# Kernel optimization log

Hardware: AMD Instinct MI355X
Metric: run time of the kernel (lower is better)

## Reference

```python
import jax, jax.numpy as jnp
import numpy as np

N = 50000       # num_node
E = 800000      # num edges (avg degree 32)
F_IN, F_HID, F_OUT = 128, 128, 64


def setup_inputs() -> dict:
    key = jax.random.key(0)
    ks = jax.random.split(key, 8)
    x = jax.random.normal(ks[0], (N, F_IN), dtype=jnp.float32)
    edge_index = jax.random.randint(ks[1], (2, E), 0, N, dtype=jnp.int64)
    edge_weight = jax.random.uniform(ks[2], (E,), dtype=jnp.float32)
    s1 = 1.0 / np.sqrt(F_IN)
    s2 = 1.0 / np.sqrt(F_HID)
    W1 = jax.random.normal(ks[3], (F_HID, F_IN), dtype=jnp.float32) * s1
    b1 = jnp.zeros((F_HID,), dtype=jnp.float32)
    W2 = jax.random.normal(ks[4], (F_HID, F_HID), dtype=jnp.float32) * s2
    b2 = jnp.zeros((F_HID,), dtype=jnp.float32)
    W3 = jax.random.normal(ks[5], (F_OUT, F_HID), dtype=jnp.float32) * s2
    b3 = jnp.zeros((F_OUT,), dtype=jnp.float32)
    return {"x": x, "edge_index": edge_index, "edge_weight": edge_weight,
            "W1": W1, "b1": b1, "W2": W2, "b2": b2, "W3": W3, "b3": b3}


def _gcn_norm(edge_index, edge_weight, num_nodes):
    # PyG gcn_norm: add self-loops (weight 1), symmetric D^-1/2 (A+I) D^-1/2
    loop = jnp.arange(num_nodes, dtype=edge_index.dtype)
    row = jnp.concatenate([edge_index[0], loop])  # source
    col = jnp.concatenate([edge_index[1], loop])  # target (aggregation index)
    ew = jnp.concatenate([edge_weight, jnp.ones((num_nodes,), edge_weight.dtype)])
    deg = jax.ops.segment_sum(ew, col, num_segments=num_nodes)
    deg_safe = jnp.where(deg > 0, deg, 1.0)
    dinv = jnp.where(deg > 0, jax.lax.rsqrt(deg_safe), 0.0)
    norm = dinv[row] * ew * dinv[col]  # [E+N]
    return row, col, norm


def reference(x, edge_index, edge_weight, W1, b1, W2, b2, W3, b3):
    num_nodes = x.shape[0]
    row, col, norm = _gcn_norm(edge_index, edge_weight, num_nodes)
    h = x
    for W, b in ((W1, b1), (W2, b2), (W3, b3)):
        m = h @ W.T                                   # [N, d_out]
        msg = m[row] * norm[:, None]                  # gather + scale, [E+N, d_out]
        agg = jax.ops.segment_sum(msg, col, num_segments=num_nodes)
        h = jax.nn.relu(agg + b)                      # GCNConv bias then ReLU
    return h.reshape(-1)                              # torch.flatten
```

## Files before the change

### kernel.cpp

```cpp
#include <hip/hip_runtime.h>
#include <hip/hip_fp16.h>


#define K_DIM 128
#define SORT_ITEMS 4096

typedef unsigned long long u64;
typedef unsigned int u32;

using half8   = __attribute__((ext_vector_type(8))) _Float16;
using floatx4 = __attribute__((ext_vector_type(4))) float;


__global__ void build_hist(const int* __restrict__ row, const int* __restrict__ col,
                           const float* __restrict__ ew, u64* __restrict__ el,
                           u32* __restrict__ ghist, int E, int N, int nb,
                           const float* __restrict__ W1, const float* __restrict__ W2,
                           const float* __restrict__ W3, __half* __restrict__ Wh,
                           int nw1, int nw2, int nw3) {
    const int b = blockIdx.x;
    if (b >= nb) {
        const int i = (b - nb) * 256 + threadIdx.x;
        const int tot = nw1 + nw2 + nw3;
        if (i < tot) {
            float v = (i < nw1) ? W1[i] : (i < nw1 + nw2 ? W2[i - nw1] : W3[i - nw1 - nw2]);
            Wh[i] = __float2half_rn(v);
        }
        return;
    }
    __shared__ u32 bin[256];
    bin[threadIdx.x] = 0;
    __syncthreads();
    const int total = E + N;
    const int base = b * SORT_ITEMS;
    const int end = min(base + SORT_ITEMS, total);
    for (int i = base + threadIdx.x; i < end; i += 256) {
        u64 e;
        if (i < E) {
            e = ((u64)(u32)col[i] << 48) | ((u64)(u32)row[i] << 32)
              | (u64)__float_as_uint(ew[i]);
        } else {
            int v = i - E;
            e = ((u64)(u32)v << 48) | ((u64)(u32)v << 32)
              | (u64)__float_as_uint(1.0f);
        }
        el[i] = e;
        atomicAdd(&bin[(u32)(e >> 56)], 1u);
    }
    __syncthreads();
    ghist[(size_t)threadIdx.x * nb + b] = bin[threadIdx.x];
}

__global__ void digit_sum(const u32* __restrict__ ghist, u32* __restrict__ dsum, int nb) {
    __shared__ u32 s[256];
    const int d = blockIdx.x;
    u32 acc = 0;
    for (int i = threadIdx.x; i < nb; i += 256) acc += ghist[(size_t)d * nb + i];
    s[threadIdx.x] = acc;
    __syncthreads();
    for (int off = 128; off > 0; off >>= 1) {
        if (threadIdx.x < off) s[threadIdx.x] += s[threadIdx.x + off];
        __syncthreads();
    }
    if (threadIdx.x == 0) dsum[d] = s[0];
}

__global__ void digit_scan(u32* __restrict__ ghist, const u32* __restrict__ dsum,
                           u32* __restrict__ dbase, int nb) {
    __shared__ u32 ds[256];
    __shared__ u32 s[256];
    const int d = blockIdx.x, t = threadIdx.x;
    ds[t] = dsum[t];
    __syncthreads();
    for (int off = 1; off < 256; off <<= 1) {
        u32 u = (t >= off) ? ds[t - off] : 0;
        __syncthreads();
        ds[t] += u;
        __syncthreads();
    }
    u32 carry = (d == 0) ? 0u : ds[d - 1];
    if (t == 0) dbase[d] = carry;
    if (d == 255 && t == 0) dbase[256] = ds[255];
    for (int base = 0; base < nb; base += 256) {
        const int i = base + t;
        const u32 v = (i < nb) ? ghist[(size_t)d * nb + i] : 0;
        s[t] = v;
        __syncthreads();
        for (int off = 1; off < 256; off <<= 1) {
            u32 u = (t >= off) ? s[t - off] : 0;
            __syncthreads();
            s[t] += u;
            __syncthreads();
        }
        if (i < nb) ghist[(size_t)d * nb + i] = carry + s[t] - v;
        carry += s[255];
        __syncthreads();
    }
}

__global__ __launch_bounds__(256) void p1_scatter(const u64* __restrict__ el,
                                                  const u32* __restrict__ ghist,
                                                  u64* __restrict__ out, int total, int nb) {
    __shared__ u32 gbase[256];
    __shared__ u32 lbase[256];
    __shared__ u32 lcur[256];
    __shared__ u64 buf[SORT_ITEMS];
    const int t = threadIdx.x;
    gbase[t] = ghist[(size_t)t * nb + blockIdx.x];
    lcur[t] = 0;
    __syncthreads();
    const int base = blockIdx.x * SORT_ITEMS;
    const int end = min(base + SORT_ITEMS, total);
    const int cnt = end - base;

    u64 it[16];
    bool ok[16];
#pragma unroll
    for (int j = 0; j < 16; ++j) {
        const int i = base + t + j * 256;
        ok[j] = i < end;
        it[j] = ok[j] ? el[i] : 0;
        if (ok[j]) atomicAdd(&lcur[(u32)(it[j] >> 56)], 1u);
    }
    __syncthreads();
    const u32 v = lcur[t];
    lbase[t] = v;
    __syncthreads();
    for (int off = 1; off < 256; off <<= 1) {
        u32 u = (t >= off) ? lbase[t - off] : 0;
        __syncthreads();
        lbase[t] += u;
        __syncthreads();
    }
    const u32 excl = lbase[t] - v;
    __syncthreads();
    lbase[t] = excl;
    lcur[t] = excl;
    __syncthreads();
#pragma unroll
    for (int j = 0; j < 16; ++j) {
        if (ok[j]) {
            const u32 d = (u32)(it[j] >> 56);
            const u32 p = atomicAdd(&lcur[d], 1u);
            buf[p] = it[j];
        }
    }
    __syncthreads();
    for (int i = t; i < cnt; i += 256) {
        const u64 e = buf[i];
        const u32 d = (u32)(e >> 56);
        out[gbase[d] + i - lbase[d]] = e;
    }
}

__global__ void p2_sort(const u64* __restrict__ in, u64* __restrict__ out,
                        const u32* __restrict__ dbase,
                        int* __restrict__ offs, float* __restrict__ dinv, int n) {
    const int t = threadIdx.x;
    const int base = (int)dbase[blockIdx.x];
    const int size = (int)dbase[blockIdx.x + 1] - base;
    __shared__ u32 hist[256], cur[256], s[256];
    __shared__ float wsum[256];
    hist[t] = 0;
    wsum[t] = 0.f;
    __syncthreads();
    for (int i = t; i < size; i += 256)
        atomicAdd(&hist[(u32)(in[base + i] >> 48) & 0xFFu], 1u);
    __syncthreads();
    const u32 v = hist[t];
    s[t] = v;
    __syncthreads();
    for (int off = 1; off < 256; off <<= 1) {
        u32 u = (t >= off) ? s[t - off] : 0;
        __syncthreads();
        s[t] += u;
        __syncthreads();
    }
    const u32 mystart = (u32)base + s[t] - v;
    cur[t] = mystart;
    __syncthreads();
    for (int i = t; i < size; i += 256) {
        u64 e = in[base + i];
        u32 lo = (u32)(e >> 48) & 0xFFu;
        u32 p = atomicAdd(&cur[lo], 1u);
        out[p] = e;
        atomicAdd(&wsum[lo], __uint_as_float((u32)(e & 0xFFFFFFFFu)));
    }
    __syncthreads();
    const int node = blockIdx.x * 256 + t;
    if (node < n && v > 0) {
        offs[node] = (int)mystart;
        dinv[node] = rsqrtf(wsum[t]);
        if (node == n - 1) offs[n] = (int)(mystart + v);
    }
}


template <int BN, bool FP32IN>
__global__ __launch_bounds__(256) void mfma_gemm(const void* __restrict__ Ain,
                                                 const __half* __restrict__ Wh,
                                                 const float* __restrict__ dinv,
                                                 __half* __restrict__ C, int nrows) {
    constexpr int NT = BN / 16;
    const int wave = threadIdx.x >> 6;
    const int lane = threadIdx.x & 63;
    const int quad = lane >> 4;
    const int l16  = lane & 15;
    const int row0 = blockIdx.x * 64 + wave * 16;

    int arow = row0 + l16;
    if (arow > nrows - 1) arow = nrows - 1;

    floatx4 acc[NT] = {};

#pragma unroll
    for (int kc = 0; kc < 4; ++kc) {
        const int kof = kc * 32 + quad * 8;
        half8 af;
        if constexpr (FP32IN) {
            const float* ap = (const float*)Ain + (size_t)arow * K_DIM + kof;
            float4 f0 = *(const float4*)ap;
            float4 f1 = *(const float4*)(ap + 4);
            af[0] = (_Float16)f0.x; af[1] = (_Float16)f0.y;
            af[2] = (_Float16)f0.z; af[3] = (_Float16)f0.w;
            af[4] = (_Float16)f1.x; af[5] = (_Float16)f1.y;
            af[6] = (_Float16)f1.z; af[7] = (_Float16)f1.w;
        } else {
            af = *(const half8*)((const __half*)Ain + (size_t)arow * K_DIM + kof);
        }
#pragma unroll
        for (int ct = 0; ct < NT; ++ct) {
            half8 bf = *(const half8*)(Wh + (size_t)(ct * 16 + l16) * K_DIM + kof);
            acc[ct] = __builtin_amdgcn_mfma_f32_16x16x32_f16(af, bf, acc[ct], 0, 0, 0);
        }
    }

    float dv[4];
    int grow[4];
    bool ok[4];
#pragma unroll
    for (int r = 0; r < 4; ++r) {
        grow[r] = row0 + quad * 4 + r;
        ok[r] = grow[r] < nrows;
        dv[r] = ok[r] ? dinv[grow[r]] : 0.f;
    }
#pragma unroll
    for (int ct = 0; ct < NT; ++ct) {
        const int colb = ct * 16 + l16;
#pragma unroll
        for (int r = 0; r < 4; ++r)
            if (ok[r])
                C[(size_t)grow[r] * BN + colb] = __float2half_rn(acc[ct][r] * dv[r]);
    }
}


template <int D, typename OUT>
__global__ __launch_bounds__(256) void agg_kernel(
    const __half* __restrict__ m, const int* __restrict__ offs,
    const int2* __restrict__ csr, const float* __restrict__ dinv,
    const float* __restrict__ bias, OUT* __restrict__ out, int n) {
    const int wid = threadIdx.x >> 6;
    const int lane = threadIdx.x & 63;
    const int node = (blockIdx.x << 2) + wid;
    if (node >= n) return;
    const int beg = offs[node];
    const int end = offs[node + 1];
    const int cnt = end - beg;
    const half8* mrow = (const half8*)m;

    const int2 ev = csr[beg + min(lane, cnt - 1)];
    const float wv = (lane < cnt) ? __int_as_float(ev.x) : 0.f;
    const int   sv = ev.y & 0xFFFF;
    const int nr = min(cnt, 64);

    float acc[8] = {0.f, 0.f, 0.f, 0.f, 0.f, 0.f, 0.f, 0.f};

    if constexpr (D == 128) {
        const int quad = lane >> 4;
        const int l16  = lane & 15;
        for (int r = 0; r * 4 < nr; ++r) {
            const int j = r * 4 + quad;
            const bool ok = j < nr;
            float w = __shfl(wv, j);
            int   s = __shfl(sv, j);
            w = ok ? w : 0.f;
            s = ok ? s : 0;
            half8 hv = mrow[(size_t)s * 16 + l16];
#pragma unroll
            for (int i = 0; i < 8; ++i)
                acc[i] = fmaf(w, (float)hv[i], acc[i]);
        }
        for (int k = beg + 64 + quad; k < end; k += 4) {
            const int2 e0 = csr[k];
            const float w0 = __int_as_float(e0.x);
            half8 hv = mrow[(size_t)(e0.y & 0xFFFF) * 16 + l16];
#pragma unroll
            for (int i = 0; i < 8; ++i)
                acc[i] = fmaf(w0, (float)hv[i], acc[i]);
        }
#pragma unroll
        for (int i = 0; i < 8; ++i) {
            acc[i] += __shfl_xor(acc[i], 16);
            acc[i] += __shfl_xor(acc[i], 32);
        }
        if (quad == 0) {
            const float dv = dinv[node];
            const float4 b0 = *(const float4*)(bias + l16 * 8);
            const float4 b1 = *(const float4*)(bias + l16 * 8 + 4);
            const float bb[8] = {b0.x, b0.y, b0.z, b0.w, b1.x, b1.y, b1.z, b1.w};
            half8 ho;
#pragma unroll
            for (int i = 0; i < 8; ++i)
                ho[i] = (_Float16)fmaxf(acc[i] * dv + bb[i], 0.f);
            *(half8*)((__half*)out + (size_t)node * 128 + l16 * 8) = ho;
        }
    } else {
        const int oct = lane >> 3;
        const int l8  = lane & 7;
        for (int r = 0; r * 8 < nr; ++r) {
            const int j = r * 8 + oct;
            const bool ok = j < nr;
            float w = __shfl(wv, j);
            int   s = __shfl(sv, j);
            w = ok ? w : 0.f;
            s = ok ? s : 0;
            half8 hv = mrow[(size_t)s * 8 + l8];
#pragma unroll
            for (int i = 0; i < 8; ++i)
                acc[i] = fmaf(w, (float)hv[i], acc[i]);
        }
        for (int k = beg + 64 + oct; k < end; k += 8) {
            const int2 e0 = csr[k];
            const float w0 = __int_as_float(e0.x);
            half8 hv = mrow[(size_t)(e0.y & 0xFFFF) * 8 + l8];
#pragma unroll
            for (int i = 0; i < 8; ++i)
                acc[i] = fmaf(w0, (float)hv[i], acc[i]);
        }
#pragma unroll
        for (int i = 0; i < 8; ++i) {
            acc[i] += __shfl_xor(acc[i], 8);
            acc[i] += __shfl_xor(acc[i], 16);
            acc[i] += __shfl_xor(acc[i], 32);
        }
        if (oct == 0) {
            const float dv = dinv[node];
            const float4 b0 = *(const float4*)(bias + l8 * 8);
            const float4 b1 = *(const float4*)(bias + l8 * 8 + 4);
            float4 v0, v1;
            v0.x = fmaxf(acc[0] * dv + b0.x, 0.f);
            v0.y = fmaxf(acc[1] * dv + b0.y, 0.f);
            v0.z = fmaxf(acc[2] * dv + b0.z, 0.f);
            v0.w = fmaxf(acc[3] * dv + b0.w, 0.f);
            v1.x = fmaxf(acc[4] * dv + b1.x, 0.f);
            v1.y = fmaxf(acc[5] * dv + b1.y, 0.f);
            v1.z = fmaxf(acc[6] * dv + b1.z, 0.f);
            v1.w = fmaxf(acc[7] * dv + b1.w, 0.f);
            float* op = (float*)out + (size_t)node * 64 + l8 * 8;
            *(float4*)op = v0;
            *(float4*)(op + 4) = v1;
        }
    }
}


extern "C" void kernel_launch(void* const* d_in, const int* in_sizes, int n_in,
                              void* d_out, int out_size, void* d_ws, size_t ws_size,
                              hipStream_t stream) {
    const float* x  = (const float*)d_in[0];
    const int*   ei = (const int*)d_in[1];
    const float* ew = (const float*)d_in[2];
    const float* W1 = (const float*)d_in[3];
    const float* b1 = (const float*)d_in[4];
    const float* W2 = (const float*)d_in[5];
    const float* b2 = (const float*)d_in[6];
    const float* W3 = (const float*)d_in[7];
    const float* b3 = (const float*)d_in[8];
    float* out = (float*)d_out;

    const int N = in_sizes[0] / K_DIM;
    const int E = in_sizes[2];
    const int* row = ei;
    const int* col = ei + E;

    const int total = E + N;
    const int nb = (total + SORT_ITEMS - 1) / SORT_ITEMS;
    const int ngroups = (N + 255) >> 8;
    const int NW1 = 128 * 128, NW2 = 128 * 128, NW3 = 64 * 128;
    const int nwb = (NW1 + NW2 + NW3 + 255) / 256;

    u64* elA      = (u64*)d_ws;
    u64* elB      = elA + total;
    __half* m_buf = (__half*)(elB + total);
    __half* h_buf = m_buf + (size_t)N * K_DIM;
    __half* Wh    = h_buf + (size_t)N * K_DIM;
    u32* ghist    = (u32*)(Wh + NW1 + NW2 + NW3);
    u32* dsum     = ghist + (size_t)256 * nb;
    u32* dbase    = dsum + 256;
    int* offs     = (int*)(dbase + 257);
    float* dinv   = (float*)(offs + N + 1);

    build_hist<<<nb + nwb, 256, 0, stream>>>(row, col, ew, elA, ghist, E, N, nb,
                                             W1, W2, W3, Wh, NW1, NW2, NW3);
    digit_sum<<<256, 256, 0, stream>>>(ghist, dsum, nb);
    digit_scan<<<256, 256, 0, stream>>>(ghist, dsum, dbase, nb);
    p1_scatter<<<nb, 256, 0, stream>>>(elA, ghist, elB, total, nb);
    p2_sort<<<ngroups, 256, 0, stream>>>(elB, elA, dbase, offs, dinv, N);

    const int gemm_blocks = (N + 63) / 64;
    const int agg_blocks = (N + 3) / 4;
    const int2* csr = (const int2*)elA;

    mfma_gemm<128, true><<<gemm_blocks, 256, 0, stream>>>(x, Wh, dinv, m_buf, N);
    agg_kernel<128, __half><<<agg_blocks, 256, 0, stream>>>(m_buf, offs, csr, dinv, b1, h_buf, N);
    mfma_gemm<128, false><<<gemm_blocks, 256, 0, stream>>>(h_buf, Wh + NW1, dinv, m_buf, N);
    agg_kernel<128, __half><<<agg_blocks, 256, 0, stream>>>(m_buf, offs, csr, dinv, b2, h_buf, N);
    mfma_gemm<64, false><<<gemm_blocks, 256, 0, stream>>>(h_buf, Wh + NW1 + NW2, dinv, m_buf, N);
    agg_kernel<64, float><<<agg_blocks, 256, 0, stream>>>(m_buf, offs, csr, dinv, b3, out, N);
}
```

Measured before the change: 282.1 us.

## Fuse layer-1 GEMM into per-bucket sort kernel and move source dinv scaling into aggregation

The first-layer GEMM no longer depends on dinv, because source-side normalization now happens in the aggregation kernels through an extra dinv[src] gather per edge. That lets the first GEMM run as extra blocks inside the second-pass sort kernel, overlapping the two independent workloads in one launch. The sort pass now uses 1024-thread blocks with four privatized histogram/weight-sum copies to cut shared atomic contention. The cost is an extra random dinv load per edge in every aggregation, and large 1024-thread blocks that may limit occupancy for the GEMM part.

```diff
diff --git a/kernel.cpp b/kernel.cpp
--- a/kernel.cpp
+++ b/kernel.cpp
@@ -153,53 +153,115 @@
     }
 }
 
-__global__ void p2_sort(const u64* __restrict__ in, u64* __restrict__ out,
-                        const u32* __restrict__ dbase,
-                        int* __restrict__ offs, float* __restrict__ dinv, int n) {
-    const int t = threadIdx.x;
-    const int base = (int)dbase[blockIdx.x];
-    const int size = (int)dbase[blockIdx.x + 1] - base;
-    __shared__ u32 hist[256], cur[256], s[256];
-    __shared__ float wsum[256];
-    hist[t] = 0;
-    wsum[t] = 0.f;
-    __syncthreads();
-    for (int i = t; i < size; i += 256)
-        atomicAdd(&hist[(u32)(in[base + i] >> 48) & 0xFFu], 1u);
-    __syncthreads();
-    const u32 v = hist[t];
-    s[t] = v;
-    __syncthreads();
-    for (int off = 1; off < 256; off <<= 1) {
-        u32 u = (t >= off) ? s[t - off] : 0;
-        __syncthreads();
-        s[t] += u;
-        __syncthreads();
-    }
-    const u32 mystart = (u32)base + s[t] - v;
-    cur[t] = mystart;
-    __syncthreads();
-    for (int i = t; i < size; i += 256) {
-        u64 e = in[base + i];
-        u32 lo = (u32)(e >> 48) & 0xFFu;
-        u32 p = atomicAdd(&cur[lo], 1u);
-        out[p] = e;
-        atomicAdd(&wsum[lo], __uint_as_float((u32)(e & 0xFFFFFFFFu)));
-    }
-    __syncthreads();
-    const int node = blockIdx.x * 256 + t;
-    if (node < n && v > 0) {
-        offs[node] = (int)mystart;
-        dinv[node] = rsqrtf(wsum[t]);
-        if (node == n - 1) offs[n] = (int)(mystart + v);
-    }
-}
-
-
-template <int BN, bool FP32IN>
-__global__ __launch_bounds__(256) void mfma_gemm(const void* __restrict__ Ain,
+__global__ __launch_bounds__(1024) void p2_gemm(
+        const u64* __restrict__ in, u64* __restrict__ out,
+        const u32* __restrict__ dbase,
+        int* __restrict__ offs, float* __restrict__ dinv, int n, int ngroups,
+        const float* __restrict__ x, const __half* __restrict__ Wh,
+        __half* __restrict__ C) {
+    if ((int)blockIdx.x < ngroups) {
+        const int t = threadIdx.x;
+        const int q = t >> 8;
+        const int b = t & 255;
+        const int base = (int)dbase[blockIdx.x];
+        const int size = (int)dbase[blockIdx.x + 1] - base;
+        __shared__ u32 hist[4][256];
+        __shared__ u32 cur[4][256];
+        __shared__ u32 s[256];
+        __shared__ float wsum[4][256];
+        hist[q][b] = 0;
+        wsum[q][b] = 0.f;
+        __syncthreads();
+        for (int i = t; i < size; i += 1024)
+            atomicAdd(&hist[q][(u32)(in[base + i] >> 48) & 0xFFu], 1u);
+        __syncthreads();
+        u32 v = 0;
+        if (t < 256) {
+            v = hist[0][b] + hist[1][b] + hist[2][b] + hist[3][b];
+            s[b] = v;
+        }
+        __syncthreads();
+        for (int off = 1; off < 256; off <<= 1) {
+            u32 u = (t < 256 && b >= off) ? s[b - off] : 0;
+            __syncthreads();
+            if (t < 256) s[b] += u;
+            __syncthreads();
+        }
+        u32 mystart = 0;
+        if (t < 256) {
+            mystart = (u32)base + s[b] - v;
+            u32 c = mystart;
+            cur[0][b] = c; c += hist[0][b];
+            cur[1][b] = c; c += hist[1][b];
+            cur[2][b] = c; c += hist[2][b];
+            cur[3][b] = c;
+        }
+        __syncthreads();
+        for (int i = t; i < size; i += 1024) {
+            u64 e = in[base + i];
+            u32 lo = (u32)(e >> 48) & 0xFFu;
+            u32 p = atomicAdd(&cur[q][lo], 1u);
+            out[p] = e;
+            atomicAdd(&wsum[q][lo], __uint_as_float((u32)(e & 0xFFFFFFFFu)));
+        }
+        __syncthreads();
+        const int node = blockIdx.x * 256 + b;
+        if (t < 256 && node < n && v > 0) {
+            offs[node] = (int)mystart;
+            dinv[node] = rsqrtf(wsum[0][b] + wsum[1][b] + wsum[2][b] + wsum[3][b]);
+            if (node == n - 1) offs[n] = (int)(mystart + v);
+        }
+    } else {
+        const int gb = blockIdx.x - ngroups;
+        const int wave = threadIdx.x >> 6;
+        const int lane = threadIdx.x & 63;
+        const int quad = lane >> 4;
+        const int l16  = lane & 15;
+        const int row0 = gb * 256 + wave * 16;
+
+        int arow = row0 + l16;
+        if (arow > n - 1) arow = n - 1;
+
+        floatx4 acc[8] = {};
+#pragma unroll
+        for (int kc = 0; kc < 4; ++kc) {
+            const int kof = kc * 32 + quad * 8;
+            const float* ap = x + (size_t)arow * K_DIM + kof;
+            float4 f0 = *(const float4*)ap;
+            float4 f1 = *(const float4*)(ap + 4);
+            half8 af;
+            af[0] = (_Float16)f0.x; af[1] = (_Float16)f0.y;
+            af[2] = (_Float16)f0.z; af[3] = (_Float16)f0.w;
+            af[4] = (_Float16)f1.x; af[5] = (_Float16)f1.y;
+            af[6] = (_Float16)f1.z; af[7] = (_Float16)f1.w;
+#pragma unroll
+            for (int ct = 0; ct < 8; ++ct) {
+                half8 bf = *(const half8*)(Wh + (size_t)(ct * 16 + l16) * K_DIM + kof);
+                acc[ct] = __builtin_amdgcn_mfma_f32_16x16x32_f16(af, bf, acc[ct], 0, 0, 0);
+            }
+        }
+        int grow[4];
+        bool ok[4];
+#pragma unroll
+        for (int r = 0; r < 4; ++r) {
+            grow[r] = row0 + quad * 4 + r;
+            ok[r] = grow[r] < n;
+        }
+#pragma unroll
+        for (int ct = 0; ct < 8; ++ct) {
+            const int colb = ct * 16 + l16;
+#pragma unroll
+            for (int r = 0; r < 4; ++r)
+                if (ok[r])
+                    C[(size_t)grow[r] * 128 + colb] = __float2half_rn(acc[ct][r]);
+        }
+    }
+}
+
+
+template <int BN>
+__global__ __launch_bounds__(256) void mfma_gemm(const __half* __restrict__ Ain,
                                                  const __half* __restrict__ Wh,
-                                                 const float* __restrict__ dinv,
                                                  __half* __restrict__ C, int nrows) {
     constexpr int NT = BN / 16;
     const int wave = threadIdx.x >> 6;
@@ -216,18 +278,7 @@
 #pragma unroll
     for (int kc = 0; kc < 4; ++kc) {
         const int kof = kc * 32 + quad * 8;
-        half8 af;
-        if constexpr (FP32IN) {
-            const float* ap = (const float*)Ain + (size_t)arow * K_DIM + kof;
-            float4 f0 = *(const float4*)ap;
-            float4 f1 = *(const float4*)(ap + 4);
-            af[0] = (_Float16)f0.x; af[1] = (_Float16)f0.y;
-            af[2] = (_Float16)f0.z; af[3] = (_Float16)f0.w;
-            af[4] = (_Float16)f1.x; af[5] = (_Float16)f1.y;
-            af[6] = (_Float16)f1.z; af[7] = (_Float16)f1.w;
-        } else {
-            af = *(const half8*)((const __half*)Ain + (size_t)arow * K_DIM + kof);
-        }
+        half8 af = *(const half8*)(Ain + (size_t)arow * K_DIM + kof);
 #pragma unroll
         for (int ct = 0; ct < NT; ++ct) {
             half8 bf = *(const half8*)(Wh + (size_t)(ct * 16 + l16) * K_DIM + kof);
@@ -235,14 +286,12 @@
         }
     }
 
-    float dv[4];
     int grow[4];
     bool ok[4];
 #pragma unroll
     for (int r = 0; r < 4; ++r) {
         grow[r] = row0 + quad * 4 + r;
         ok[r] = grow[r] < nrows;
-        dv[r] = ok[r] ? dinv[grow[r]] : 0.f;
     }
 #pragma unroll
     for (int ct = 0; ct < NT; ++ct) {
@@ -250,7 +299,7 @@
 #pragma unroll
         for (int r = 0; r < 4; ++r)
             if (ok[r])
-                C[(size_t)grow[r] * BN + colb] = __float2half_rn(acc[ct][r] * dv[r]);
+                C[(size_t)grow[r] * BN + colb] = __float2half_rn(acc[ct][r]);
     }
 }
 
@@ -270,8 +319,9 @@
     const half8* mrow = (const half8*)m;
 
     const int2 ev = csr[beg + min(lane, cnt - 1)];
-    const float wv = (lane < cnt) ? __int_as_float(ev.x) : 0.f;
     const int   sv = ev.y & 0xFFFF;
+    const float ds = dinv[sv];
+    const float wv = (lane < cnt) ? __int_as_float(ev.x) * ds : 0.f;
     const int nr = min(cnt, 64);
 
     float acc[8] = {0.f, 0.f, 0.f, 0.f, 0.f, 0.f, 0.f, 0.f};
@@ -293,8 +343,9 @@
         }
         for (int k = beg + 64 + quad; k < end; k += 4) {
             const int2 e0 = csr[k];
-            const float w0 = __int_as_float(e0.x);
-            half8 hv = mrow[(size_t)(e0.y & 0xFFFF) * 16 + l16];
+            const int  s0 = e0.y & 0xFFFF;
+            const float w0 = __int_as_float(e0.x) * dinv[s0];
+            half8 hv = mrow[(size_t)s0 * 16 + l16];
 #pragma unroll
             for (int i = 0; i < 8; ++i)
                 acc[i] = fmaf(w0, (float)hv[i], acc[i]);
@@ -332,8 +383,9 @@
         }
         for (int k = beg + 64 + oct; k < end; k += 8) {
             const int2 e0 = csr[k];
-            const float w0 = __int_as_float(e0.x);
-            half8 hv = mrow[(size_t)(e0.y & 0xFFFF) * 8 + l8];
+            const int  s0 = e0.y & 0xFFFF;
+            const float w0 = __int_as_float(e0.x) * dinv[s0];
+            half8 hv = mrow[(size_t)s0 * 8 + l8];
 #pragma unroll
             for (int i = 0; i < 8; ++i)
                 acc[i] = fmaf(w0, (float)hv[i], acc[i]);
@@ -406,16 +458,18 @@
     digit_sum<<<256, 256, 0, stream>>>(ghist, dsum, nb);
     digit_scan<<<256, 256, 0, stream>>>(ghist, dsum, dbase, nb);
     p1_scatter<<<nb, 256, 0, stream>>>(elA, ghist, elB, total, nb);
-    p2_sort<<<ngroups, 256, 0, stream>>>(elB, elA, dbase, offs, dinv, N);
+
+    const int gemm1_blocks = (N + 255) / 256;
+    p2_gemm<<<ngroups + gemm1_blocks, 1024, 0, stream>>>(
+        elB, elA, dbase, offs, dinv, N, ngroups, x, Wh, m_buf);
 
     const int gemm_blocks = (N + 63) / 64;
     const int agg_blocks = (N + 3) / 4;
     const int2* csr = (const int2*)elA;
 
-    mfma_gemm<128, true><<<gemm_blocks, 256, 0, stream>>>(x, Wh, dinv, m_buf, N);
     agg_kernel<128, __half><<<agg_blocks, 256, 0, stream>>>(m_buf, offs, csr, dinv, b1, h_buf, N);
-    mfma_gemm<128, false><<<gemm_blocks, 256, 0, stream>>>(h_buf, Wh + NW1, dinv, m_buf, N);
+    mfma_gemm<128><<<gemm_blocks, 256, 0, stream>>>(h_buf, Wh + NW1, m_buf, N);
     agg_kernel<128, __half><<<agg_blocks, 256, 0, stream>>>(m_buf, offs, csr, dinv, b2, h_buf, N);
-    mfma_gemm<64, false><<<gemm_blocks, 256, 0, stream>>>(h_buf, Wh + NW1 + NW2, dinv, m_buf, N);
+    mfma_gemm<64><<<gemm_blocks, 256, 0, stream>>>(h_buf, Wh + NW1 + NW2, m_buf, N);
     agg_kernel<64, float><<<agg_blocks, 256, 0, stream>>>(m_buf, offs, csr, dinv, b3, out, N);
 }
```

Measured after the change: 274.6 us. -2.6%, faster.
